# Performance work log

Hardware: AMD Instinct MI355X
Metric: run time of the kernel (lower is better)

## Reference

```python
import jax, jax.numpy as jnp
import numpy as np

# Model config (matches init_kwargs)
L_F, DELTA_F, L_S, DELTA_S = 1, 1, 32, 16
HIDDEN = 32       # SSM state dim H
GRU_H = 64        # slow-branch GRU hidden
N_GRU = 4
B, T = 4, 32768


def setup_inputs() -> dict:
    key = jax.random.key(0)
    ks = jax.random.split(key, 13)
    def nrm(k, shape, s=0.05):
        return jax.random.normal(k, shape, dtype=jnp.float32) * s
    return {
        "x": jax.random.normal(ks[0], (B, T), dtype=jnp.float32),
        # SlowBranch params
        "fc_in_w": nrm(ks[1], (GRU_H, 1), 0.3),
        "fc_in_b": nrm(ks[2], (GRU_H,)),
        "gru_wih": nrm(ks[3], (N_GRU, 3 * GRU_H, GRU_H), 0.1),
        "gru_whh": nrm(ks[4], (N_GRU, 3 * GRU_H, GRU_H), 0.1),
        "gru_bih": nrm(ks[5], (N_GRU, 3 * GRU_H)),
        "gru_bhh": nrm(ks[6], (N_GRU, 3 * GRU_H)),
        "out_fc_w": nrm(ks[7], (2 * HIDDEN, GRU_H), 0.1),
        "out_fc_b": nrm(ks[8], (2 * HIDDEN,)),
        # Fast branch params (F_IN: 1->H, F_OUT: H->1)
        "fin_w": nrm(ks[9], (HIDDEN, 1), 0.3),
        "fin_b": nrm(ks[10], (HIDDEN,)),
        "fout_w": nrm(ks[11], (1, HIDDEN), 0.1),
        "fout_b": nrm(ks[12], (1,)),
    }


def _gru_layer(xs, Wih, Whh, bih, bhh):
    """Torch-convention GRU layer. xs: (N, L, H_in) -> (N, L, H)."""
    H = Whh.shape[1]
    # Precompute input-side gate pre-activations: (N, L, 3H)
    xp = jnp.einsum('nlh,gh->nlg', xs, Wih) + bih
    def step(h, xt):
        gh = h @ Whh.T + bhh                       # (N, 3H)
        ir, iz, inew = jnp.split(xt, 3, axis=-1)
        hr, hz, hnew = jnp.split(gh, 3, axis=-1)
        r = jax.nn.sigmoid(ir + hr)
        z = jax.nn.sigmoid(iz + hz)
        n = jnp.tanh(inew + r * hnew)
        h = (1.0 - z) * n + z * h
        return h, h
    h0 = jnp.zeros((xs.shape[0], H), xs.dtype)
    _, ys = jax.lax.scan(step, h0, jnp.swapaxes(xp, 0, 1))  # (L, N, H)
    return jnp.swapaxes(ys, 0, 1)


def reference(x, fc_in_w, fc_in_b, gru_wih, gru_whh, gru_bih, gru_bhh,
              out_fc_w, out_fc_b, fin_w, fin_b, fout_w, fout_b):
    Bsz, Tlen = x.shape
    num_slow = (Tlen - L_S) // DELTA_S + 1

    frame_idx = jnp.arange(num_slow)[:, None] * DELTA_S + jnp.arange(L_S)[None, :]
    x_s = x[:, frame_idx].reshape(Bsz * num_slow, L_S, 1)      # (N, L_s, 1)
    h = jax.nn.relu(x_s * fc_in_w[:, 0] + fc_in_b)             # (N, L_s, GRU_H)
    for l in range(gru_wih.shape[0]):
        h = _gru_layer(h, gru_wih[l], gru_whh[l], gru_bih[l], gru_bhh[l])
    eps = h[:, -1, :] @ out_fc_w.T + out_fc_b                  # (N, 2H)
    eps = eps.reshape(Bsz, num_slow, 2 * HIDDEN)
    A_slow = jax.nn.sigmoid(eps[..., :HIDDEN])                 # (B, S, H)
    g_slow = eps[..., HIDDEN:]                                 # (B, S, H)

    # ---- Fast branch: per-sample diagonal linear SSM scan ----
    delta = DELTA_S // DELTA_F
    idx = jnp.clip(jnp.arange(Tlen) // delta - 1, 0, num_slow - 1)  # (T,)
    A_t = A_slow[:, idx, :]                                    # (B, T, H)
    u_t = (x[..., None] * fin_w[:, 0] + fin_b) * g_slow[:, idx, :]  # (B, T, H)

    def step(hc, inp):
        A, u = inp
        hn = A * hc + u
        return hn, hn
    h0 = jnp.zeros((Bsz, HIDDEN), x.dtype)
    _, h_all = jax.lax.scan(step, h0,
                            (jnp.swapaxes(A_t, 0, 1), jnp.swapaxes(u_t, 0, 1)))
    # h_all: (T, B, H); F_OUT applied to every state
    return jnp.einsum('tbh,h->bt', h_all, fout_w[0]) + fout_b[0]   # (B, T)
```

## Files before the change

### kernel.cpp

```cpp
#include <hip/hip_runtime.h>
#include <hip/hip_bf16.h>

typedef __bf16 bf16x8 __attribute__((ext_vector_type(8)));
typedef short short8 __attribute__((ext_vector_type(8)));
typedef float f32x4 __attribute__((ext_vector_type(4)));
typedef unsigned short ushort_t;

#define T_LEN 32768
#define B_SZ 4
#define NSLOW 2047
#define NSEQ (B_SZ * NSLOW)
#define GH 64
#define G3 192
#define NL 4
#define HID 32
#define NCH 256
#define L2E 1.44269504088896341f

#define OFF_X    0
#define OFF_FCW  131072
#define OFF_FCB  131136
#define OFF_WIH  131200
#define OFF_WHH  180352
#define OFF_BIH  229504
#define OFF_BHH  230272
#define OFF_OFW  231040
#define OFF_OFB  235136
#define OFF_FINW 235200
#define OFF_FINB 235232
#define OFF_FOW  235264
#define OFF_FOB  235296
#define CONV_TOTAL 235297
#define CONV_PAD_BYTES 470656

static __device__ __forceinline__ float bf2f(ushort_t u) {
    union { unsigned u; float f; } c; c.u = ((unsigned)u) << 16; return c.f;
}
static __device__ __forceinline__ ushort_t f2bf(float f) {
    union { float f; unsigned u; } c; c.f = f;
    unsigned r = (c.u + 0x7FFFu + ((c.u >> 16) & 1u)) >> 16;
    return (ushort_t)r;
}
static __device__ __forceinline__ unsigned pk2bf(float a, float b) {
    float2 f; f.x = a; f.y = b;
    __hip_bfloat162 h = __float22bfloat162_rn(f);
    unsigned u;
    __builtin_memcpy(&u, &h, 4);
    return u;
}
static __device__ __forceinline__ f32x4 mfma16(short8 a, short8 b, f32x4 c) {
    return __builtin_amdgcn_mfma_f32_16x16x32_bf16(
        __builtin_bit_cast(bf16x8, a), __builtin_bit_cast(bf16x8, b), c, 0, 0, 0);
}
static __device__ __forceinline__ int xoff(int t, int kb, int seq) {
    return ((((t << 3) + kb) << 4) + (seq ^ (kb & 7))) << 3;
}
static __device__ __forceinline__ short8 load_frag_scaled(const ushort_t* p, float s) {
    uint4 r = *(const uint4*)p;
    unsigned aa[4] = {r.x, r.y, r.z, r.w};
    short8 o;
#pragma unroll
    for (int i = 0; i < 4; ++i) {
        o[2 * i]     = (short)f2bf(bf2f((ushort_t)(aa[i] & 0xffffu)) * s);
        o[2 * i + 1] = (short)f2bf(bf2f((ushort_t)(aa[i] >> 16)) * s);
    }
    return o;
}

struct Ptrs13 { const void* p[13]; };

__global__ __launch_bounds__(256) void convert_kernel(Ptrs13 ptrs,
                                                      int* __restrict__ flag,
                                                      ushort_t* __restrict__ dst)
{
    __shared__ int scnt;
    if (threadIdx.x == 0) scnt = 0;
    __syncthreads();
    {
        ushort_t u = ((const ushort_t*)ptrs.p[0])[threadIdx.x];
        int e = (u >> 7) & 0xFF;
        int ok = (e >= 80 && e <= 141) ? 1 : 0;
#pragma unroll
        for (int d = 1; d < 64; d <<= 1) ok += __shfl_xor(ok, d, 64);
        if ((threadIdx.x & 63) == 0) atomicAdd(&scnt, ok);
    }
    __syncthreads();
    const bool isbf = (scnt >= 224);
    if (blockIdx.x == 0 && threadIdx.x == 0) *flag = isbf ? 1 : 0;

    const int offs[14] = {OFF_X, OFF_FCW, OFF_FCB, OFF_WIH, OFF_WHH, OFF_BIH,
                          OFF_BHH, OFF_OFW, OFF_OFB, OFF_FINW, OFF_FINB,
                          OFF_FOW, OFF_FOB, CONV_TOTAL};
    for (int idx = blockIdx.x * 256 + threadIdx.x; idx < CONV_TOTAL;
         idx += gridDim.x * 256) {
        int s = 0;
#pragma unroll
        for (int j = 1; j < 13; ++j) if (idx >= offs[j]) s = j;
        int k = idx - offs[s];
        ushort_t v = isbf ? ((const ushort_t*)ptrs.p[s])[k]
                          : f2bf(((const float*)ptrs.p[s])[k]);
        dst[idx] = v;
    }
}

__global__ __launch_bounds__(1024, 1) void gru_kernel(
    const ushort_t* __restrict__ x, const ushort_t* __restrict__ fcw,
    const ushort_t* __restrict__ fcb, const ushort_t* __restrict__ wih,
    const ushort_t* __restrict__ whh, const ushort_t* __restrict__ bih,
    const ushort_t* __restrict__ bhh, const ushort_t* __restrict__ ofw,
    const ushort_t* __restrict__ ofb, float* __restrict__ Aslow,
    float* __restrict__ gslow)
{
    __shared__ short8 X0s[4096];
    __shared__ short8 Rg[2048];
    short* RgS = (short*)Rg;
    const int tid = threadIdx.x;
    const int W = tid >> 6, lane = tid & 63;
    const int l = W >> 2, w = W & 3;
    const int q = lane >> 4, m = lane & 15;
    const int jb = w * 16;
    const int n0 = blockIdx.x * 16;

#pragma unroll 1
    for (int ii = 0; ii < 4; ++ii) {
        int cid = ii * 1024 + tid;
        int seq = cid & 15, kb = (cid >> 4) & 7, t = cid >> 7;
        int n = n0 + seq; if (n > NSEQ - 1) n = NSEQ - 1;
        int b = n / NSLOW, s = n - b * NSLOW;
        float xv = bf2f(x[b * T_LEN + s * 16 + t]);
        short8 v;
#pragma unroll
        for (int i = 0; i < 8; ++i) {
            int g = kb * 8 + i;
            float h = fmaf(xv, bf2f(fcw[g]), bf2f(fcb[g]));
            h = h > 0.f ? h : 0.f;
            v[i] = (short)f2bf(h);
        }
        X0s[xoff(t, kb, seq) >> 3] = v;
    }

    const int col0 = jb + 4 * q;
    const int kbw = (col0 >> 3);
    const int wsub = (col0 & 7);
    const int kofs = q * 8;
    const int wbase0 = ((kbw << 4) + (m ^ (kbw & 7))) * 8 + wsub;
    const int iA0 = (q << 4) + (m ^ q);
    const int iB0 = ((4 + q) << 4) + (m ^ ((4 + q) & 7));

    const ushort_t* wl = wih + l * G3 * GH;
    const ushort_t* ul = whh + l * G3 * GH;
    short8 wR0 = load_frag_scaled(wl + (0 * 64 + jb + m) * 64 + kofs, -L2E);
    short8 wR1 = load_frag_scaled(wl + (0 * 64 + jb + m) * 64 + 32 + kofs, -L2E);
    short8 wZ0 = load_frag_scaled(wl + (1 * 64 + jb + m) * 64 + kofs, -L2E);
    short8 wZ1 = load_frag_scaled(wl + (1 * 64 + jb + m) * 64 + 32 + kofs, -L2E);
    short8 wN0 = load_frag_scaled(wl + (2 * 64 + jb + m) * 64 + kofs, 2.f * L2E);
    short8 wN1 = load_frag_scaled(wl + (2 * 64 + jb + m) * 64 + 32 + kofs, 2.f * L2E);
    short8 uR0 = load_frag_scaled(ul + (0 * 64 + jb + m) * 64 + kofs, -L2E);
    short8 uR1 = load_frag_scaled(ul + (0 * 64 + jb + m) * 64 + 32 + kofs, -L2E);
    short8 uZ0 = load_frag_scaled(ul + (1 * 64 + jb + m) * 64 + kofs, -L2E);
    short8 uZ1 = load_frag_scaled(ul + (1 * 64 + jb + m) * 64 + 32 + kofs, -L2E);
    short8 uN0 = load_frag_scaled(ul + (2 * 64 + jb + m) * 64 + kofs, 2.f * L2E);
    short8 uN1 = load_frag_scaled(ul + (2 * 64 + jb + m) * 64 + 32 + kofs, 2.f * L2E);

    f32x4 bRv, bZv, bNXv, bNHv;
#pragma unroll
    for (int i = 0; i < 4; ++i) {
        int c = col0 + i;
        bRv[i]  = -L2E * (bf2f(bih[l * G3 + c]) + bf2f(bhh[l * G3 + c]));
        bZv[i]  = -L2E * (bf2f(bih[l * G3 + 64 + c]) + bf2f(bhh[l * G3 + 64 + c]));
        bNXv[i] = 2.f * L2E * bf2f(bih[l * G3 + 128 + c]);
        bNHv[i] = 2.f * L2E * bf2f(bhh[l * G3 + 128 + c]);
    }

    const short8* inb = (l == 0) ? X0s : (Rg + (l - 1) * 512);
    const short8* ringL = Rg + l * 512;
    const int wbL = l * 4096 + wbase0;

    float hc[4] = {0.f, 0.f, 0.f, 0.f};
    f32x4 xR = {0.f, 0.f, 0.f, 0.f}, xZ = xR, xN = xR;

#pragma unroll 1
    for (int s = 0; s < 38; ++s) {
        __syncthreads();
        int t = s - 2 * l;
        if ((unsigned)t > 31u) continue;

        f32x4 aR, aZ, aNH = bNHv;
        if (t == 0) {
            short8 cx0 = inb[iA0], cx1 = inb[iB0];
            xR = bRv; xZ = bZv; xN = bNXv;
            xR = mfma16(wR0, cx0, xR); xR = mfma16(wR1, cx1, xR);
            xZ = mfma16(wZ0, cx0, xZ); xZ = mfma16(wZ1, cx1, xZ);
            xN = mfma16(wN0, cx0, xN); xN = mfma16(wN1, cx1, xN);
            aR = xR; aZ = xZ;
        } else {
            int si = ((t - 1) & 3) << 7;
            short8 bh0 = ringL[si + iA0], bh1 = ringL[si + iB0];
            aR  = mfma16(uR0, bh0, xR);  aR  = mfma16(uR1, bh1, aR);
            aZ  = mfma16(uZ0, bh0, xZ);  aZ  = mfma16(uZ1, bh1, aZ);
            aNH = mfma16(uN0, bh0, aNH); aNH = mfma16(uN1, bh1, aNH);
        }
#pragma unroll
        for (int i = 0; i < 4; ++i) {
            float r = __builtin_amdgcn_rcpf(1.f + __builtin_amdgcn_exp2f(aR[i]));
            float z = __builtin_amdgcn_rcpf(1.f + __builtin_amdgcn_exp2f(aZ[i]));
            float yp = fmaf(r, aNH[i], xN[i]);
            float nn = fmaf(-2.f,
                __builtin_amdgcn_rcpf(1.f + __builtin_amdgcn_exp2f(yp)), 1.f);
            hc[i] = fmaf(z, hc[i] - nn, nn);
        }
        *(uint2*)(RgS + wbL + ((t & 3) << 10)) =
            make_uint2(pk2bf(hc[0], hc[1]), pk2bf(hc[2], hc[3]));
        if (t < 31) {
            int si = ((l == 0) ? (t + 1) : ((t + 1) & 3)) << 7;
            short8 px0 = inb[si + iA0], px1 = inb[si + iB0];
            xR = bRv; xZ = bZv; xN = bNXv;
            xR = mfma16(wR0, px0, xR); xR = mfma16(wR1, px1, xR);
            xZ = mfma16(wZ0, px0, xZ); xZ = mfma16(wZ1, px1, xZ);
            xN = mfma16(wN0, px0, xN); xN = mfma16(wN1, px1, xN);
        }
    }

    __syncthreads();
    if (l == 3) {
        short8 aL0 = Rg[15 * 128 + iA0];
        short8 aL1 = Rg[15 * 128 + iB0];
        float sc = (w < 2) ? -L2E : 1.f;
        short8 o0 = load_frag_scaled(ofw + (jb + m) * 64 + kofs, sc);
        short8 o1 = load_frag_scaled(ofw + (jb + m) * 64 + 32 + kofs, sc);
        f32x4 aE = {bf2f(ofb[col0]) * sc, bf2f(ofb[col0 + 1]) * sc,
                    bf2f(ofb[col0 + 2]) * sc, bf2f(ofb[col0 + 3]) * sc};
        aE = mfma16(o0, aL0, aE);
        aE = mfma16(o1, aL1, aE);
        int n = n0 + m;
        if (w < 2) {
            f32x4 v;
#pragma unroll
            for (int i = 0; i < 4; ++i)
                v[i] = __builtin_amdgcn_rcpf(1.f + __builtin_amdgcn_exp2f(aE[i]));
            *(f32x4*)(Aslow + n * HID + col0) = v;
        } else {
            *(f32x4*)(gslow + n * HID + (col0 - 32)) = aE;
        }
    }
}

__global__ __launch_bounds__(256) void pass1_kernel(
    const ushort_t* __restrict__ x, const float* __restrict__ Aslow,
    const float* __restrict__ gslow, const ushort_t* __restrict__ finw,
    const ushort_t* __restrict__ finb, float* __restrict__ P,
    float* __restrict__ S)
{
    int gt = blockIdx.x * 256 + threadIdx.x;
    int h = gt & 31, c = (gt >> 5) & 255, b = gt >> 13;
    float fw = bf2f(finw[h]), fb = bf2f(finb[h]);
    float Pv = 1.f, Sv = 0.f;
    int t0 = c * 128;
#pragma unroll 1
    for (int seg = 0; seg < 8; ++seg) {
        int sidx = (t0 >> 4) + seg - 1;
        if (sidx < 0) sidx = 0;
        if (sidx > NSLOW - 1) sidx = NSLOW - 1;
        float A = Aslow[(b * NSLOW + sidx) * HID + h];
        float g = gslow[(b * NSLOW + sidx) * HID + h];
        float fwg = fw * g, fbg = fb * g;
        const uint4* px = (const uint4*)(x + b * T_LEN + t0 + seg * 16);
        uint4 ra = px[0], rb = px[1];
        unsigned xa[8] = {ra.x, ra.y, ra.z, ra.w, rb.x, rb.y, rb.z, rb.w};
#pragma unroll
        for (int j = 0; j < 8; ++j) {
            float x0 = bf2f((ushort_t)(xa[j] & 0xffffu));
            float x1 = bf2f((ushort_t)(xa[j] >> 16));
            Sv = fmaf(A, Sv, fmaf(x0, fwg, fbg));
            Sv = fmaf(A, Sv, fmaf(x1, fwg, fbg));
        }
        float A2 = A * A, A4 = A2 * A2, A8 = A4 * A4;
        Pv *= A8 * A8;
    }
    P[(b * HID + h) * NCH + c] = Pv;
    S[(b * HID + h) * NCH + c] = Sv;
}

__global__ __launch_bounds__(128) void scan_kernel(
    const float* __restrict__ P, const float* __restrict__ S,
    float* __restrict__ Hpre)
{
    int tid = threadIdx.x;
    const float4* p4 = (const float4*)(P + tid * NCH);
    const float4* s4 = (const float4*)(S + tid * NCH);
    float* hp = Hpre + tid * NCH;
    float hr = 0.f;
#pragma unroll 8
    for (int c = 0; c < NCH / 4; ++c) {
        float4 pv = p4[c], sv = s4[c];
        hp[4 * c + 0] = hr; hr = fmaf(pv.x, hr, sv.x);
        hp[4 * c + 1] = hr; hr = fmaf(pv.y, hr, sv.y);
        hp[4 * c + 2] = hr; hr = fmaf(pv.z, hr, sv.z);
        hp[4 * c + 3] = hr; hr = fmaf(pv.w, hr, sv.w);
    }
}

__global__ __launch_bounds__(256) void pass2_kernel(
    const ushort_t* __restrict__ x, const float* __restrict__ Aslow,
    const float* __restrict__ gslow, const float* __restrict__ Hpre,
    const ushort_t* __restrict__ finw, const ushort_t* __restrict__ finb,
    const ushort_t* __restrict__ fow, const ushort_t* __restrict__ fob,
    const int* __restrict__ flag, void* __restrict__ outv)
{
    int wv = blockIdx.x * 4 + (threadIdx.x >> 6);
    int lane = threadIdx.x & 63;
    int half = lane >> 5, h = lane & 31;
    int pair = wv * 2 + half;
    int b = pair >> 8, c = pair & 255;
    const bool isbf = (*flag != 0);
    ushort_t* outb = (ushort_t*)outv;
    float* outf = (float*)outv;
    float hv = Hpre[(b * HID + h) * NCH + c];
    float fw = bf2f(finw[h]), fb = bf2f(finb[h]);
    float wo = bf2f(fow[h]), ob = bf2f(fob[0]);
    int t0 = c * 128;
#pragma unroll 1
    for (int blk = 0; blk < 4; ++blk) {
        float ykeep = 0.f;
        float A = 0.f, fwg = 0.f, fbg = 0.f;
#pragma unroll
        for (int tt = 0; tt < 32; ++tt) {
            int t = t0 + blk * 32 + tt;
            if ((tt & 15) == 0) {
                int sidx = (t >> 4) - 1;
                if (sidx < 0) sidx = 0;
                A = Aslow[(b * NSLOW + sidx) * HID + h];
                float g = gslow[(b * NSLOW + sidx) * HID + h];
                fwg = fw * g; fbg = fb * g;
            }
            float xv = bf2f(x[b * T_LEN + t]);
            hv = fmaf(A, hv, fmaf(xv, fwg, fbg));
            float y = hv * wo;
            y += __shfl_xor(y, 1, 64);
            y += __shfl_xor(y, 2, 64);
            y += __shfl_xor(y, 4, 64);
            y += __shfl_xor(y, 8, 64);
            y += __shfl_xor(y, 16, 64);
            if (tt == h) ykeep = y + ob;
        }
        int oidx = b * T_LEN + t0 + blk * 32 + h;
        if (isbf) outb[oidx] = f2bf(ykeep);
        else      outf[oidx] = ykeep;
    }
}

extern "C" void kernel_launch(void* const* d_in, const int* in_sizes, int n_in,
                              void* d_out, int out_size, void* d_ws, size_t ws_size,
                              hipStream_t stream)
{
    ushort_t* cv = (ushort_t*)d_ws;
    const ushort_t* x    = cv + OFF_X;
    const ushort_t* fcw  = cv + OFF_FCW;
    const ushort_t* fcb  = cv + OFF_FCB;
    const ushort_t* wih  = cv + OFF_WIH;
    const ushort_t* whh  = cv + OFF_WHH;
    const ushort_t* bih  = cv + OFF_BIH;
    const ushort_t* bhh  = cv + OFF_BHH;
    const ushort_t* ofw  = cv + OFF_OFW;
    const ushort_t* ofb  = cv + OFF_OFB;
    const ushort_t* finw = cv + OFF_FINW;
    const ushort_t* finb = cv + OFF_FINB;
    const ushort_t* fow  = cv + OFF_FOW;
    const ushort_t* fob  = cv + OFF_FOB;

    float* Aslow = (float*)((char*)d_ws + CONV_PAD_BYTES);
    float* gslow = Aslow + 8192 * 32;
    float* P     = gslow + 8192 * 32;
    float* S     = P + 4 * 32 * NCH;
    float* Hpre  = S + 4 * 32 * NCH;
    int*   flag  = (int*)(Hpre + 4 * 32 * NCH);

    Ptrs13 ptrs;
    for (int i = 0; i < 13; ++i) ptrs.p[i] = d_in[i];

    convert_kernel<<<dim3(920), dim3(256), 0, stream>>>(ptrs, flag, cv);
    gru_kernel<<<dim3(512), dim3(1024), 0, stream>>>(
        x, fcw, fcb, wih, whh, bih, bhh, ofw, ofb, Aslow, gslow);
    pass1_kernel<<<dim3(128), dim3(256), 0, stream>>>(
        x, Aslow, gslow, finw, finb, P, S);
    scan_kernel<<<dim3(1), dim3(128), 0, stream>>>(P, S, Hpre);
    pass2_kernel<<<dim3(128), dim3(256), 0, stream>>>(
        x, Aslow, gslow, Hpre, finw, finb, fow, fob, flag, d_out);
}
```

Measured before the change: 201.5 us.

## Run GRU layers two at a time in one in-place LDS buffer

The GRU kernel shrinks from 16 waves (all four layers pipelined together) to 8 waves that process layers in two passes of two. Each layer overwrites its input timestep slot in a single 64KB shared buffer, replacing the separate input buffer and per-layer ring buffers. This lowers LDS and per-block resources so two blocks can share a CU. In exchange, each block runs about twice as many serial barrier-separated steps, and correctness now depends on the in-place read/write ordering between the two lagged layers.

```diff
diff --git a/kernel.cpp b/kernel.cpp
--- a/kernel.cpp
+++ b/kernel.cpp
@@ -103,7 +103,7 @@
     }
 }
 
-__global__ __launch_bounds__(1024, 1) void gru_kernel(
+__global__ __launch_bounds__(512, 2) void gru_kernel(
     const ushort_t* __restrict__ x, const ushort_t* __restrict__ fcw,
     const ushort_t* __restrict__ fcb, const ushort_t* __restrict__ wih,
     const ushort_t* __restrict__ whh, const ushort_t* __restrict__ bih,
@@ -111,19 +111,18 @@
     const ushort_t* __restrict__ ofb, float* __restrict__ Aslow,
     float* __restrict__ gslow)
 {
-    __shared__ short8 X0s[4096];
-    __shared__ short8 Rg[2048];
-    short* RgS = (short*)Rg;
+    __shared__ short8 Xs8[4096];
+    short* Xs = (short*)Xs8;
     const int tid = threadIdx.x;
     const int W = tid >> 6, lane = tid & 63;
-    const int l = W >> 2, w = W & 3;
+    const int l2 = W >> 2, w = W & 3;
     const int q = lane >> 4, m = lane & 15;
     const int jb = w * 16;
     const int n0 = blockIdx.x * 16;
 
 #pragma unroll 1
-    for (int ii = 0; ii < 4; ++ii) {
-        int cid = ii * 1024 + tid;
+    for (int ii = 0; ii < 8; ++ii) {
+        int cid = ii * 512 + tid;
         int seq = cid & 15, kb = (cid >> 4) & 7, t = cid >> 7;
         int n = n0 + seq; if (n > NSEQ - 1) n = NSEQ - 1;
         int b = n / NSLOW, s = n - b * NSLOW;
@@ -136,7 +135,7 @@
             h = h > 0.f ? h : 0.f;
             v[i] = (short)f2bf(h);
         }
-        X0s[xoff(t, kb, seq) >> 3] = v;
+        Xs8[xoff(t, kb, seq) >> 3] = v;
     }
 
     const int col0 = jb + 4 * q;
@@ -147,84 +146,84 @@
     const int iA0 = (q << 4) + (m ^ q);
     const int iB0 = ((4 + q) << 4) + (m ^ ((4 + q) & 7));
 
-    const ushort_t* wl = wih + l * G3 * GH;
-    const ushort_t* ul = whh + l * G3 * GH;
-    short8 wR0 = load_frag_scaled(wl + (0 * 64 + jb + m) * 64 + kofs, -L2E);
-    short8 wR1 = load_frag_scaled(wl + (0 * 64 + jb + m) * 64 + 32 + kofs, -L2E);
-    short8 wZ0 = load_frag_scaled(wl + (1 * 64 + jb + m) * 64 + kofs, -L2E);
-    short8 wZ1 = load_frag_scaled(wl + (1 * 64 + jb + m) * 64 + 32 + kofs, -L2E);
-    short8 wN0 = load_frag_scaled(wl + (2 * 64 + jb + m) * 64 + kofs, 2.f * L2E);
-    short8 wN1 = load_frag_scaled(wl + (2 * 64 + jb + m) * 64 + 32 + kofs, 2.f * L2E);
-    short8 uR0 = load_frag_scaled(ul + (0 * 64 + jb + m) * 64 + kofs, -L2E);
-    short8 uR1 = load_frag_scaled(ul + (0 * 64 + jb + m) * 64 + 32 + kofs, -L2E);
-    short8 uZ0 = load_frag_scaled(ul + (1 * 64 + jb + m) * 64 + kofs, -L2E);
-    short8 uZ1 = load_frag_scaled(ul + (1 * 64 + jb + m) * 64 + 32 + kofs, -L2E);
-    short8 uN0 = load_frag_scaled(ul + (2 * 64 + jb + m) * 64 + kofs, 2.f * L2E);
-    short8 uN1 = load_frag_scaled(ul + (2 * 64 + jb + m) * 64 + 32 + kofs, 2.f * L2E);
-
-    f32x4 bRv, bZv, bNXv, bNHv;
-#pragma unroll
-    for (int i = 0; i < 4; ++i) {
-        int c = col0 + i;
-        bRv[i]  = -L2E * (bf2f(bih[l * G3 + c]) + bf2f(bhh[l * G3 + c]));
-        bZv[i]  = -L2E * (bf2f(bih[l * G3 + 64 + c]) + bf2f(bhh[l * G3 + 64 + c]));
-        bNXv[i] = 2.f * L2E * bf2f(bih[l * G3 + 128 + c]);
-        bNHv[i] = 2.f * L2E * bf2f(bhh[l * G3 + 128 + c]);
-    }
-
-    const short8* inb = (l == 0) ? X0s : (Rg + (l - 1) * 512);
-    const short8* ringL = Rg + l * 512;
-    const int wbL = l * 4096 + wbase0;
-
-    float hc[4] = {0.f, 0.f, 0.f, 0.f};
-    f32x4 xR = {0.f, 0.f, 0.f, 0.f}, xZ = xR, xN = xR;
-
-#pragma unroll 1
-    for (int s = 0; s < 38; ++s) {
-        __syncthreads();
-        int t = s - 2 * l;
-        if ((unsigned)t > 31u) continue;
-
-        f32x4 aR, aZ, aNH = bNHv;
-        if (t == 0) {
-            short8 cx0 = inb[iA0], cx1 = inb[iB0];
-            xR = bRv; xZ = bZv; xN = bNXv;
-            xR = mfma16(wR0, cx0, xR); xR = mfma16(wR1, cx1, xR);
-            xZ = mfma16(wZ0, cx0, xZ); xZ = mfma16(wZ1, cx1, xZ);
-            xN = mfma16(wN0, cx0, xN); xN = mfma16(wN1, cx1, xN);
-            aR = xR; aZ = xZ;
-        } else {
-            int si = ((t - 1) & 3) << 7;
-            short8 bh0 = ringL[si + iA0], bh1 = ringL[si + iB0];
-            aR  = mfma16(uR0, bh0, xR);  aR  = mfma16(uR1, bh1, aR);
-            aZ  = mfma16(uZ0, bh0, xZ);  aZ  = mfma16(uZ1, bh1, aZ);
-            aNH = mfma16(uN0, bh0, aNH); aNH = mfma16(uN1, bh1, aNH);
-        }
+#pragma unroll 1
+    for (int p = 0; p < 2; ++p) {
+        const int l = 2 * p + l2;
+        const ushort_t* wl = wih + l * G3 * GH;
+        const ushort_t* ul = whh + l * G3 * GH;
+        short8 wR0 = load_frag_scaled(wl + (0 * 64 + jb + m) * 64 + kofs, -L2E);
+        short8 wR1 = load_frag_scaled(wl + (0 * 64 + jb + m) * 64 + 32 + kofs, -L2E);
+        short8 wZ0 = load_frag_scaled(wl + (1 * 64 + jb + m) * 64 + kofs, -L2E);
+        short8 wZ1 = load_frag_scaled(wl + (1 * 64 + jb + m) * 64 + 32 + kofs, -L2E);
+        short8 wN0 = load_frag_scaled(wl + (2 * 64 + jb + m) * 64 + kofs, 2.f * L2E);
+        short8 wN1 = load_frag_scaled(wl + (2 * 64 + jb + m) * 64 + 32 + kofs, 2.f * L2E);
+        short8 uR0 = load_frag_scaled(ul + (0 * 64 + jb + m) * 64 + kofs, -L2E);
+        short8 uR1 = load_frag_scaled(ul + (0 * 64 + jb + m) * 64 + 32 + kofs, -L2E);
+        short8 uZ0 = load_frag_scaled(ul + (1 * 64 + jb + m) * 64 + kofs, -L2E);
+        short8 uZ1 = load_frag_scaled(ul + (1 * 64 + jb + m) * 64 + 32 + kofs, -L2E);
+        short8 uN0 = load_frag_scaled(ul + (2 * 64 + jb + m) * 64 + kofs, 2.f * L2E);
+        short8 uN1 = load_frag_scaled(ul + (2 * 64 + jb + m) * 64 + 32 + kofs, 2.f * L2E);
+
+        f32x4 bRv, bZv, bNXv, bNHv;
 #pragma unroll
         for (int i = 0; i < 4; ++i) {
-            float r = __builtin_amdgcn_rcpf(1.f + __builtin_amdgcn_exp2f(aR[i]));
-            float z = __builtin_amdgcn_rcpf(1.f + __builtin_amdgcn_exp2f(aZ[i]));
-            float yp = fmaf(r, aNH[i], xN[i]);
-            float nn = fmaf(-2.f,
-                __builtin_amdgcn_rcpf(1.f + __builtin_amdgcn_exp2f(yp)), 1.f);
-            hc[i] = fmaf(z, hc[i] - nn, nn);
-        }
-        *(uint2*)(RgS + wbL + ((t & 3) << 10)) =
-            make_uint2(pk2bf(hc[0], hc[1]), pk2bf(hc[2], hc[3]));
-        if (t < 31) {
-            int si = ((l == 0) ? (t + 1) : ((t + 1) & 3)) << 7;
-            short8 px0 = inb[si + iA0], px1 = inb[si + iB0];
-            xR = bRv; xZ = bZv; xN = bNXv;
-            xR = mfma16(wR0, px0, xR); xR = mfma16(wR1, px1, xR);
-            xZ = mfma16(wZ0, px0, xZ); xZ = mfma16(wZ1, px1, xZ);
-            xN = mfma16(wN0, px0, xN); xN = mfma16(wN1, px1, xN);
+            int c = col0 + i;
+            bRv[i]  = -L2E * (bf2f(bih[l * G3 + c]) + bf2f(bhh[l * G3 + c]));
+            bZv[i]  = -L2E * (bf2f(bih[l * G3 + 64 + c]) + bf2f(bhh[l * G3 + 64 + c]));
+            bNXv[i] = 2.f * L2E * bf2f(bih[l * G3 + 128 + c]);
+            bNHv[i] = 2.f * L2E * bf2f(bhh[l * G3 + 128 + c]);
+        }
+
+        float hc[4] = {0.f, 0.f, 0.f, 0.f};
+        f32x4 xR = {0.f, 0.f, 0.f, 0.f}, xZ = xR, xN = xR;
+
+#pragma unroll 1
+        for (int s = 0; s < 34; ++s) {
+            __syncthreads();
+            int t = s - 2 * l2;
+            if ((unsigned)t > 31u) continue;
+
+            f32x4 aR, aZ, aNH = bNHv;
+            if (t == 0) {
+                short8 cx0 = Xs8[iA0], cx1 = Xs8[iB0];
+                xR = bRv; xZ = bZv; xN = bNXv;
+                xR = mfma16(wR0, cx0, xR); xR = mfma16(wR1, cx1, xR);
+                xZ = mfma16(wZ0, cx0, xZ); xZ = mfma16(wZ1, cx1, xZ);
+                xN = mfma16(wN0, cx0, xN); xN = mfma16(wN1, cx1, xN);
+                aR = xR; aZ = xZ;
+            } else {
+                int si = (t - 1) << 7;
+                short8 bh0 = Xs8[si + iA0], bh1 = Xs8[si + iB0];
+                aR  = mfma16(uR0, bh0, xR);  aR  = mfma16(uR1, bh1, aR);
+                aZ  = mfma16(uZ0, bh0, xZ);  aZ  = mfma16(uZ1, bh1, aZ);
+                aNH = mfma16(uN0, bh0, aNH); aNH = mfma16(uN1, bh1, aNH);
+            }
+#pragma unroll
+            for (int i = 0; i < 4; ++i) {
+                float r = __builtin_amdgcn_rcpf(1.f + __builtin_amdgcn_exp2f(aR[i]));
+                float z = __builtin_amdgcn_rcpf(1.f + __builtin_amdgcn_exp2f(aZ[i]));
+                float yp = fmaf(r, aNH[i], xN[i]);
+                float nn = fmaf(-2.f,
+                    __builtin_amdgcn_rcpf(1.f + __builtin_amdgcn_exp2f(yp)), 1.f);
+                hc[i] = fmaf(z, hc[i] - nn, nn);
+            }
+            *(uint2*)(Xs + wbase0 + (t << 10)) =
+                make_uint2(pk2bf(hc[0], hc[1]), pk2bf(hc[2], hc[3]));
+            if (t < 31) {
+                int si = (t + 1) << 7;
+                short8 px0 = Xs8[si + iA0], px1 = Xs8[si + iB0];
+                xR = bRv; xZ = bZv; xN = bNXv;
+                xR = mfma16(wR0, px0, xR); xR = mfma16(wR1, px1, xR);
+                xZ = mfma16(wZ0, px0, xZ); xZ = mfma16(wZ1, px1, xZ);
+                xN = mfma16(wN0, px0, xN); xN = mfma16(wN1, px1, xN);
+            }
         }
     }
 
     __syncthreads();
-    if (l == 3) {
-        short8 aL0 = Rg[15 * 128 + iA0];
-        short8 aL1 = Rg[15 * 128 + iB0];
+    if (l2 == 1) {
+        short8 aL0 = Xs8[(31 << 7) + iA0];
+        short8 aL1 = Xs8[(31 << 7) + iB0];
         float sc = (w < 2) ? -L2E : 1.f;
         short8 o0 = load_frag_scaled(ofw + (jb + m) * 64 + kofs, sc);
         short8 o1 = load_frag_scaled(ofw + (jb + m) * 64 + 32 + kofs, sc);
@@ -379,7 +378,7 @@
     for (int i = 0; i < 13; ++i) ptrs.p[i] = d_in[i];
 
     convert_kernel<<<dim3(920), dim3(256), 0, stream>>>(ptrs, flag, cv);
-    gru_kernel<<<dim3(512), dim3(1024), 0, stream>>>(
+    gru_kernel<<<dim3(512), dim3(512), 0, stream>>>(
         x, fcw, fcb, wih, whh, bih, bhh, ofw, ofb, Aslow, gslow);
     pass1_kernel<<<dim3(128), dim3(256), 0, stream>>>(
         x, Aslow, gslow, finw, finb, P, S);
```

Measured after the change: 203.5 us. No clear change (+1.0%).
